# Optimization experiments

Measured on AMD Instinct MI355X. Metric: run time of the kernel, lower is better.

Reference implementation:

```python
import jax, jax.numpy as jnp
import numpy as np

VOCAB, DIM = 100000, 512
BATCH, SEQ = 4096, 200
HID, OUT = 256, 20


def setup_inputs() -> dict:
    key = jax.random.key(0)
    k_emb, k_x, k_len, k_w1, k_b1, k_w2, k_b2 = jax.random.split(key, 7)
    emb_table = jax.random.normal(k_emb, (VOCAB, DIM), dtype=jnp.float32) * 0.1
    x = jax.random.randint(k_x, (BATCH, SEQ), 0, VOCAB, dtype=jnp.int64)
    # lengths in [1, SEQ] to avoid division by zero, matching real padded batches
    lengths = jax.random.randint(k_len, (BATCH,), 1, SEQ + 1, dtype=jnp.int64)
    bows = jnp.zeros((BATCH,), dtype=jnp.float32)  # unused by the model's forward
    # Linear(2*DIM, 256) and Linear(256, OUT); stored transposed for x @ W
    W1 = jax.random.normal(k_w1, (2 * DIM, HID), dtype=jnp.float32) * (1.0 / np.sqrt(2 * DIM))
    b1 = jax.random.normal(k_b1, (HID,), dtype=jnp.float32) * 0.01
    W2 = jax.random.normal(k_w2, (HID, OUT), dtype=jnp.float32) * (1.0 / np.sqrt(HID))
    b2 = jax.random.normal(k_b2, (OUT,), dtype=jnp.float32) * 0.01
    return {"emb_table": emb_table, "W1": W1, "b1": b1, "W2": W2, "b2": b2,
            "x": x, "lengths": lengths, "bows": bows}


def reference(emb_table, W1, b1, W2, b2, x, lengths, bows):
    # Gather: [B, S, D]
    emb = emb_table[x]
    # Faithful to original: sum over the FULL sequence (padding included),
    # divided by the true length; max also over the full sequence.
    rep_mean = jnp.sum(emb, axis=1) / lengths.astype(emb.dtype)[:, None]  # [B, D]
    rep_max = jnp.max(emb, axis=1)                                        # [B, D]
    rep = jnp.concatenate([rep_mean, rep_max], axis=1)                    # [B, 2D]
    h = jax.nn.relu(rep @ W1 + b1)                                        # [B, 256]
    logits = h @ W2 + b2                                                  # [B, OUT]
    return logits
```

## Files before the change

kernel.cpp:

```cpp
#include <hip/hip_runtime.h>
#include <hip/hip_bf16.h>

#define VOCAB 100000
#define DIM   512
#define BATCH 4096
#define SEQ   200
#define HID   256
#define OUTN  20

typedef __attribute__((ext_vector_type(8))) short short8;
typedef __attribute__((ext_vector_type(4))) float floatx4;

static __device__ __forceinline__ unsigned short f2bf(float f) {
    __hip_bfloat16 b = __float2bfloat16(f);
    return *(unsigned short*)&b;
}
static __device__ __forceinline__ float bf2f(unsigned short u) {
    unsigned int v = (unsigned int)u << 16;
    return *(float*)&v;
}

__global__ __launch_bounds__(256) void k_cvt(
    const float* __restrict__ src, unsigned short* __restrict__ dst)
{
    const int n8 = VOCAB * DIM / 8;
    int i = blockIdx.x * 256 + threadIdx.x;
    const int stride = gridDim.x * 256;
    const float4* s4 = (const float4*)src;
    short8* d8 = (short8*)dst;
    for (; i < n8; i += stride) {
        const float4 a = s4[2 * i];
        const float4 b = s4[2 * i + 1];
        short8 o;
        o[0] = (short)f2bf(a.x); o[1] = (short)f2bf(a.y);
        o[2] = (short)f2bf(a.z); o[3] = (short)f2bf(a.w);
        o[4] = (short)f2bf(b.x); o[5] = (short)f2bf(b.y);
        o[6] = (short)f2bf(b.z); o[7] = (short)f2bf(b.w);
        d8[i] = o;
    }
}

__global__ __launch_bounds__(128) void k_reduce_bf(
    const unsigned short* __restrict__ embb, const int* __restrict__ x,
    const int* __restrict__ lengths, unsigned short* __restrict__ repb)
{
    const int b = blockIdx.x;
    const int t = threadIdx.x;
    const int w = t >> 6;
    const int lane = t & 63;

    __shared__ int sidx[SEQ];
    for (int i = t; i < SEQ; i += 128) sidx[i] = x[b * SEQ + i];
    __syncthreads();

    float s[8] = {0.f, 0.f, 0.f, 0.f, 0.f, 0.f, 0.f, 0.f};
    float m[8] = {-1e30f, -1e30f, -1e30f, -1e30f, -1e30f, -1e30f, -1e30f, -1e30f};

    const unsigned short* base = embb + lane * 8;
    const int i0 = w * (SEQ / 2);

#pragma unroll 4
    for (int i = i0; i < i0 + SEQ / 2; ++i) {
        const short8 v = *(const short8*)(base + (size_t)sidx[i] * DIM);
#pragma unroll
        for (int j = 0; j < 8; ++j) {
            const float f = bf2f((unsigned short)v[j]);
            s[j] += f;
            m[j] = fmaxf(m[j], f);
        }
    }

    __shared__ float red[2][2][DIM];
#pragma unroll
    for (int j = 0; j < 8; ++j) {
        red[w][0][lane * 8 + j] = s[j];
        red[w][1][lane * 8 + j] = m[j];
    }
    __syncthreads();

    const float inv = 1.0f / (float)lengths[b];
    const int c0 = t * 4;
    unsigned long long mu = 0, xu = 0;
#pragma unroll
    for (int j = 0; j < 4; ++j) {
        const float sv = red[0][0][c0 + j] + red[1][0][c0 + j];
        const float mv = fmaxf(red[0][1][c0 + j], red[1][1][c0 + j]);
        mu |= (unsigned long long)f2bf(sv * inv) << (16 * j);
        xu |= (unsigned long long)f2bf(mv)       << (16 * j);
    }
    unsigned short* row = repb + (size_t)b * (2 * DIM);
    *(unsigned long long*)(row + c0)       = mu;
    *(unsigned long long*)(row + DIM + c0) = xu;
}

__global__ __launch_bounds__(128) void k_reduce(
    const float* __restrict__ emb, const int* __restrict__ x,
    const int* __restrict__ lengths, unsigned short* __restrict__ repb)
{
    const int b = blockIdx.x;
    const int t = threadIdx.x;

    __shared__ int sidx[SEQ];
    for (int i = t; i < SEQ; i += 128) sidx[i] = x[b * SEQ + i];
    __syncthreads();

    const float4* embv = (const float4*)emb;
    float4 s = make_float4(0.f, 0.f, 0.f, 0.f);
    float4 m = make_float4(-1e30f, -1e30f, -1e30f, -1e30f);

#pragma unroll 4
    for (int i = 0; i < SEQ; ++i) {
        const float4 v = embv[(size_t)sidx[i] * (DIM / 4) + t];
        s.x += v.x; s.y += v.y; s.z += v.z; s.w += v.w;
        m.x = fmaxf(m.x, v.x); m.y = fmaxf(m.y, v.y);
        m.z = fmaxf(m.z, v.z); m.w = fmaxf(m.w, v.w);
    }

    const float inv = 1.0f / (float)lengths[b];
    unsigned long long mu =
          (unsigned long long)f2bf(s.x * inv)
        | ((unsigned long long)f2bf(s.y * inv) << 16)
        | ((unsigned long long)f2bf(s.z * inv) << 32)
        | ((unsigned long long)f2bf(s.w * inv) << 48);
    unsigned long long xu =
          (unsigned long long)f2bf(m.x)
        | ((unsigned long long)f2bf(m.y) << 16)
        | ((unsigned long long)f2bf(m.z) << 32)
        | ((unsigned long long)f2bf(m.w) << 48);

    unsigned short* row = repb + (size_t)b * (2 * DIM);
    *(unsigned long long*)(row + 4 * t)       = mu;
    *(unsigned long long*)(row + DIM + 4 * t) = xu;
}

__global__ __launch_bounds__(256) void k_w1t(
    const float* __restrict__ W1, unsigned short* __restrict__ W1T)
{
    __shared__ unsigned short s[64][65];
    const int n0 = blockIdx.x * 64;
    const int k0 = blockIdx.y * 64;
    const int t = threadIdx.x;

#pragma unroll
    for (int i = 0; i < 4; ++i) {
        const int kk = (t >> 4) + i * 16;
        const int cc = (t & 15) * 4;
        const float4 v = *(const float4*)&W1[(size_t)(k0 + kk) * HID + n0 + cc];
        s[cc + 0][kk] = f2bf(v.x);
        s[cc + 1][kk] = f2bf(v.y);
        s[cc + 2][kk] = f2bf(v.z);
        s[cc + 3][kk] = f2bf(v.w);
    }
    __syncthreads();

#pragma unroll
    for (int i = 0; i < 4; ++i) {
        const int nn = (t >> 4) + i * 16;
        const int kq = (t & 15) * 4;
        unsigned long long u =
              (unsigned long long)s[nn][kq + 0]
            | ((unsigned long long)s[nn][kq + 1] << 16)
            | ((unsigned long long)s[nn][kq + 2] << 32)
            | ((unsigned long long)s[nn][kq + 3] << 48);
        *(unsigned long long*)&W1T[(size_t)(n0 + nn) * (2 * DIM) + k0 + kq] = u;
    }
}

#define APAD 40

__global__ __launch_bounds__(256) void k_gemm1(
    const unsigned short* __restrict__ repb,
    const unsigned short* __restrict__ w1t,
    const float* __restrict__ bias, float* __restrict__ h)
{
    const int K = 2 * DIM;
    const int rowBase = blockIdx.y * 64;
    const int colBase = blockIdx.x * 64;
    const int tid  = threadIdx.x;
    const int lane = tid & 63;
    const int wv   = tid >> 6;
    const int wm   = wv & 1;
    const int wn   = wv >> 1;

    __shared__ unsigned short sA[64][APAD];
    __shared__ unsigned short sB[64][APAD];

    const int r  = tid >> 2;
    const int kq = tid & 3;

    const unsigned short* gA = repb + (size_t)(rowBase + r) * K + kq * 8;
    const unsigned short* gB = w1t  + (size_t)(colBase + r) * K + kq * 8;

    floatx4 acc[2][2] = {{{0.f,0.f,0.f,0.f},{0.f,0.f,0.f,0.f}},
                         {{0.f,0.f,0.f,0.f},{0.f,0.f,0.f,0.f}}};

    short8 pa = *(const short8*)gA;
    short8 pb = *(const short8*)gB;

    const int lm = lane & 15;
    const int lq = lane >> 4;
    for (int k0 = 0; k0 < K; k0 += 32) {
        __syncthreads();
        *(short8*)&sA[r][kq * 8] = pa;
        *(short8*)&sB[r][kq * 8] = pb;
        __syncthreads();

        if (k0 + 32 < K) {
            pa = *(const short8*)(gA + k0 + 32);
            pb = *(const short8*)(gB + k0 + 32);
        }

        const short8 a0 = *(const short8*)&sA[wm * 32 + lm][lq * 8];
        const short8 a1 = *(const short8*)&sA[wm * 32 + 16 + lm][lq * 8];
        const short8 b0 = *(const short8*)&sB[wn * 32 + lm][lq * 8];
        const short8 b1 = *(const short8*)&sB[wn * 32 + 16 + lm][lq * 8];

        acc[0][0] = __builtin_amdgcn_mfma_f32_16x16x32_bf16(a0, b0, acc[0][0], 0, 0, 0);
        acc[0][1] = __builtin_amdgcn_mfma_f32_16x16x32_bf16(a0, b1, acc[0][1], 0, 0, 0);
        acc[1][0] = __builtin_amdgcn_mfma_f32_16x16x32_bf16(a1, b0, acc[1][0], 0, 0, 0);
        acc[1][1] = __builtin_amdgcn_mfma_f32_16x16x32_bf16(a1, b1, acc[1][1], 0, 0, 0);
    }

#pragma unroll
    for (int nt = 0; nt < 2; ++nt) {
        const int col = colBase + wn * 32 + nt * 16 + lm;
        const float bb = bias[col];
#pragma unroll
        for (int mt = 0; mt < 2; ++mt) {
#pragma unroll
            for (int rg = 0; rg < 4; ++rg) {
                const int row = rowBase + wm * 32 + mt * 16 + lq * 4 + rg;
                h[(size_t)row * HID + col] = fmaxf(acc[mt][nt][rg] + bb, 0.f);
            }
        }
    }
}

#define R3 32
#define HPAD 260

__global__ __launch_bounds__(256) void k_gemm2(
    const float* __restrict__ H, const float* __restrict__ W2,
    const float* __restrict__ b2, float* __restrict__ outp)
{
    __shared__ float sh[R3 * HPAD];
    __shared__ float sw[HID * OUTN];
    __shared__ float sb[OUTN];

    const int t = threadIdx.x;
    const int rowBase = blockIdx.x * R3;

    const float4* H4 = (const float4*)H;
    for (int i = t; i < R3 * (HID / 4); i += 256) {
        const int r  = i >> 6;
        const int c4 = i & 63;
        *(float4*)&sh[r * HPAD + c4 * 4] = H4[(size_t)(rowBase + r) * (HID / 4) + c4];
    }
    for (int i = t; i < HID * OUTN; i += 256) sw[i] = W2[i];
    if (t < OUTN) sb[t] = b2[t];
    __syncthreads();

    for (int o = t; o < R3 * OUTN; o += 256) {
        const int r = o / OUTN;
        const int c = o - r * OUTN;
        float acc = sb[c];
#pragma unroll 8
        for (int k = 0; k < HID; ++k)
            acc += sh[r * HPAD + k] * sw[k * OUTN + c];
        outp[(size_t)(rowBase + r) * OUTN + c] = acc;
    }
}

extern "C" void kernel_launch(void* const* d_in, const int* in_sizes, int n_in,
                              void* d_out, int out_size, void* d_ws, size_t ws_size,
                              hipStream_t stream)
{
    const float* emb     = (const float*)d_in[0];
    const float* W1      = (const float*)d_in[1];
    const float* b1      = (const float*)d_in[2];
    const float* W2      = (const float*)d_in[3];
    const float* b2      = (const float*)d_in[4];
    const int*   x       = (const int*)d_in[5];
    const int*   lengths = (const int*)d_in[6];

    float* out = (float*)d_out;

    const size_t embbN = (size_t)VOCAB * DIM;
    const size_t repbN = (size_t)BATCH * 2 * DIM;
    const size_t w1tN  = (size_t)HID * 2 * DIM;
    const size_t hN    = (size_t)BATCH * HID;
    const size_t needFast = (embbN + repbN + w1tN) * 2 + hN * 4 + 256;

    if (ws_size >= needFast) {
        unsigned short* embb = (unsigned short*)d_ws;
        unsigned short* repb = embb + embbN;
        unsigned short* w1t  = repb + repbN;
        float* h = (float*)(w1t + w1tN);

        k_cvt<<<2048, 256, 0, stream>>>(emb, embb);
        k_w1t<<<dim3(HID / 64, (2 * DIM) / 64), 256, 0, stream>>>(W1, w1t);
        k_reduce_bf<<<BATCH, 128, 0, stream>>>(embb, x, lengths, repb);
        k_gemm1<<<dim3(HID / 64, BATCH / 64), 256, 0, stream>>>(repb, w1t, b1, h);
        k_gemm2<<<BATCH / R3, 256, 0, stream>>>(h, W2, b2, out);
    } else {
        unsigned short* repb = (unsigned short*)d_ws;
        unsigned short* w1t  = repb + repbN;
        float* h = (float*)(w1t + w1tN);

        k_w1t<<<dim3(HID / 64, (2 * DIM) / 64), 256, 0, stream>>>(W1, w1t);
        k_reduce<<<BATCH, 128, 0, stream>>>(emb, x, lengths, repb);
        k_gemm1<<<dim3(HID / 64, BATCH / 64), 256, 0, stream>>>(repb, w1t, b1, h);
        k_gemm2<<<BATCH / R3, 256, 0, stream>>>(h, W2, b2, out);
    }
}
```

Before: 441.9 us.

## Widen reduce blocks to four waves, nontemporal cvt loads, restructure gemm2 with transposed W2

The bf16 gather-reduce kernel now runs four wavefronts per batch row, each covering a quarter of the sequence, with a four-way shared-memory combine at the end. The fp32-to-bf16 conversion uses nontemporal loads so the streamed table is less likely to evict useful cache lines. The small second GEMM transposes W2 into padded shared memory and gives each thread one row and up to three output columns, using float4 dot products in place of scalar strided reads. The aim is more memory-level parallelism in the gather and less shared-memory traffic in gemm2. The cost is more shared memory and synchronisation per block in the reduce kernel.

```diff
diff --git a/kernel.cpp b/kernel.cpp
--- a/kernel.cpp
+++ b/kernel.cpp
@@ -26,21 +26,21 @@
     const int n8 = VOCAB * DIM / 8;
     int i = blockIdx.x * 256 + threadIdx.x;
     const int stride = gridDim.x * 256;
-    const float4* s4 = (const float4*)src;
+    const floatx4* s4 = (const floatx4*)src;
     short8* d8 = (short8*)dst;
     for (; i < n8; i += stride) {
-        const float4 a = s4[2 * i];
-        const float4 b = s4[2 * i + 1];
+        const floatx4 a = __builtin_nontemporal_load(&s4[2 * i]);
+        const floatx4 b = __builtin_nontemporal_load(&s4[2 * i + 1]);
         short8 o;
-        o[0] = (short)f2bf(a.x); o[1] = (short)f2bf(a.y);
-        o[2] = (short)f2bf(a.z); o[3] = (short)f2bf(a.w);
-        o[4] = (short)f2bf(b.x); o[5] = (short)f2bf(b.y);
-        o[6] = (short)f2bf(b.z); o[7] = (short)f2bf(b.w);
+        o[0] = (short)f2bf(a[0]); o[1] = (short)f2bf(a[1]);
+        o[2] = (short)f2bf(a[2]); o[3] = (short)f2bf(a[3]);
+        o[4] = (short)f2bf(b[0]); o[5] = (short)f2bf(b[1]);
+        o[6] = (short)f2bf(b[2]); o[7] = (short)f2bf(b[3]);
         d8[i] = o;
     }
 }
 
-__global__ __launch_bounds__(128) void k_reduce_bf(
+__global__ __launch_bounds__(256) void k_reduce_bf(
     const unsigned short* __restrict__ embb, const int* __restrict__ x,
     const int* __restrict__ lengths, unsigned short* __restrict__ repb)
 {
@@ -50,17 +50,17 @@
     const int lane = t & 63;
 
     __shared__ int sidx[SEQ];
-    for (int i = t; i < SEQ; i += 128) sidx[i] = x[b * SEQ + i];
+    for (int i = t; i < SEQ; i += 256) sidx[i] = x[b * SEQ + i];
     __syncthreads();
 
     float s[8] = {0.f, 0.f, 0.f, 0.f, 0.f, 0.f, 0.f, 0.f};
     float m[8] = {-1e30f, -1e30f, -1e30f, -1e30f, -1e30f, -1e30f, -1e30f, -1e30f};
 
     const unsigned short* base = embb + lane * 8;
-    const int i0 = w * (SEQ / 2);
-
-#pragma unroll 4
-    for (int i = i0; i < i0 + SEQ / 2; ++i) {
+    const int i0 = w * (SEQ / 4);
+
+#pragma unroll 5
+    for (int i = i0; i < i0 + SEQ / 4; ++i) {
         const short8 v = *(const short8*)(base + (size_t)sidx[i] * DIM);
 #pragma unroll
         for (int j = 0; j < 8; ++j) {
@@ -70,7 +70,7 @@
         }
     }
 
-    __shared__ float red[2][2][DIM];
+    __shared__ float red[4][2][DIM];
 #pragma unroll
     for (int j = 0; j < 8; ++j) {
         red[w][0][lane * 8 + j] = s[j];
@@ -79,18 +79,20 @@
     __syncthreads();
 
     const float inv = 1.0f / (float)lengths[b];
-    const int c0 = t * 4;
-    unsigned long long mu = 0, xu = 0;
-#pragma unroll
-    for (int j = 0; j < 4; ++j) {
-        const float sv = red[0][0][c0 + j] + red[1][0][c0 + j];
-        const float mv = fmaxf(red[0][1][c0 + j], red[1][1][c0 + j]);
-        mu |= (unsigned long long)f2bf(sv * inv) << (16 * j);
-        xu |= (unsigned long long)f2bf(mv)       << (16 * j);
+    const int c0 = t * 2;
+    unsigned int mu = 0, xu = 0;
+#pragma unroll
+    for (int j = 0; j < 2; ++j) {
+        const float sv = red[0][0][c0 + j] + red[1][0][c0 + j]
+                       + red[2][0][c0 + j] + red[3][0][c0 + j];
+        const float mv = fmaxf(fmaxf(red[0][1][c0 + j], red[1][1][c0 + j]),
+                               fmaxf(red[2][1][c0 + j], red[3][1][c0 + j]));
+        mu |= (unsigned int)f2bf(sv * inv) << (16 * j);
+        xu |= (unsigned int)f2bf(mv)       << (16 * j);
     }
     unsigned short* row = repb + (size_t)b * (2 * DIM);
-    *(unsigned long long*)(row + c0)       = mu;
-    *(unsigned long long*)(row + DIM + c0) = xu;
+    *(unsigned int*)(row + c0)       = mu;
+    *(unsigned int*)(row + DIM + c0) = xu;
 }
 
 __global__ __launch_bounds__(128) void k_reduce(
@@ -237,14 +239,14 @@
 }
 
 #define R3 32
-#define HPAD 260
+#define HP4 260
 
 __global__ __launch_bounds__(256) void k_gemm2(
     const float* __restrict__ H, const float* __restrict__ W2,
     const float* __restrict__ b2, float* __restrict__ outp)
 {
-    __shared__ float sh[R3 * HPAD];
-    __shared__ float sw[HID * OUTN];
+    __shared__ float sh[R3][HP4];
+    __shared__ float swt[OUTN][HP4];
     __shared__ float sb[OUTN];
 
     const int t = threadIdx.x;
@@ -254,21 +256,38 @@
     for (int i = t; i < R3 * (HID / 4); i += 256) {
         const int r  = i >> 6;
         const int c4 = i & 63;
-        *(float4*)&sh[r * HPAD + c4 * 4] = H4[(size_t)(rowBase + r) * (HID / 4) + c4];
-    }
-    for (int i = t; i < HID * OUTN; i += 256) sw[i] = W2[i];
+        *(float4*)&sh[r][c4 * 4] = H4[(size_t)(rowBase + r) * (HID / 4) + c4];
+    }
+    {
+        const int k = t;
+#pragma unroll
+        for (int c = 0; c < OUTN; ++c) swt[c][k] = W2[k * OUTN + c];
+    }
     if (t < OUTN) sb[t] = b2[t];
     __syncthreads();
 
-    for (int o = t; o < R3 * OUTN; o += 256) {
-        const int r = o / OUTN;
-        const int c = o - r * OUTN;
-        float acc = sb[c];
+    const int r  = t & 31;
+    const int cs = t >> 5;
+    float a0 = sb[cs], a1 = sb[cs + 8], a2 = (cs + 16 < OUTN) ? sb[cs + 16] : 0.f;
+    float acc0 = 0.f, acc1 = 0.f, acc2 = 0.f;
+
 #pragma unroll 8
-        for (int k = 0; k < HID; ++k)
-            acc += sh[r * HPAD + k] * sw[k * OUTN + c];
-        outp[(size_t)(rowBase + r) * OUTN + c] = acc;
-    }
+    for (int k = 0; k < HID; k += 4) {
+        const float4 a = *(const float4*)&sh[r][k];
+        const float4 w0 = *(const float4*)&swt[cs][k];
+        const float4 w1 = *(const float4*)&swt[cs + 8][k];
+        acc0 += a.x * w0.x + a.y * w0.y + a.z * w0.z + a.w * w0.w;
+        acc1 += a.x * w1.x + a.y * w1.y + a.z * w1.z + a.w * w1.w;
+        if (cs + 16 < OUTN) {
+            const float4 w2 = *(const float4*)&swt[cs + 16][k];
+            acc2 += a.x * w2.x + a.y * w2.y + a.z * w2.z + a.w * w2.w;
+        }
+    }
+
+    float* orow = outp + (size_t)(rowBase + r) * OUTN;
+    orow[cs]     = acc0 + a0;
+    orow[cs + 8] = acc1 + a1;
+    if (cs + 16 < OUTN) orow[cs + 16] = acc2 + a2;
 }
 
 extern "C" void kernel_launch(void* const* d_in, const int* in_sizes, int n_in,
@@ -299,7 +318,7 @@
 
         k_cvt<<<2048, 256, 0, stream>>>(emb, embb);
         k_w1t<<<dim3(HID / 64, (2 * DIM) / 64), 256, 0, stream>>>(W1, w1t);
-        k_reduce_bf<<<BATCH, 128, 0, stream>>>(embb, x, lengths, repb);
+        k_reduce_bf<<<BATCH, 256, 0, stream>>>(embb, x, lengths, repb);
         k_gemm1<<<dim3(HID / 64, BATCH / 64), 256, 0, stream>>>(repb, w1t, b1, h);
         k_gemm2<<<BATCH / R3, 256, 0, stream>>>(h, W2, b2, out);
     } else {
```

New measurement: 424.9 us. -3.8%, faster.
